# Kernel tuning notes

Hardware: AMD Instinct MI355X
Metric: run time of the kernel (lower is better)

## Reference

```python
import jax, jax.numpy as jnp
import numpy as np

B, S, D, K = 4, 4096, 1024, 64

def setup_inputs() -> dict:
    key = jax.random.key(0)
    kx, kq, kk, kv, ko = jax.random.split(key, 5)
    scale = 1.0 / np.sqrt(D)
    return {
        "x": jax.random.normal(kx, (B, S, D), dtype=jnp.float32),
        "Wq": jax.random.uniform(kq, (K, D), dtype=jnp.float32, minval=-scale, maxval=scale),
        "Wk": jax.random.uniform(kk, (K, D), dtype=jnp.float32, minval=-scale, maxval=scale),
        "Wv": jax.random.uniform(kv, (K, D), dtype=jnp.float32, minval=-scale, maxval=scale),
        "Wo": jax.random.uniform(ko, (D, K), dtype=jnp.float32, minval=-1.0/np.sqrt(K), maxval=1.0/np.sqrt(K)),
    }

def reference(x, Wq, Wk, Wv, Wo):
    # projections: torch Linear(dim, key_dim, bias=False) -> x @ W.T
    Q = jax.nn.elu(x @ Wq.T) + 1.0          # [B,S,K]
    Kf = jax.nn.elu(x @ Wk.T) + 1.0         # [B,S,K]
    V = x @ Wv.T                             # [B,S,K]
    # causal running KV state via cumsum of outer products: [B,S,K,K]
    KV_sum = jnp.cumsum(Kf[..., :, None] * V[..., None, :], axis=1)
    K_sum = jnp.cumsum(Kf, axis=1)           # [B,S,K]
    num = jnp.einsum('bsk,bskm->bsm', Q, KV_sum)   # [B,S,K]
    den = jnp.einsum('bsk,bsk->bs', Q, K_sum)[..., None]
    out = num / (den + 1e-6)
    return out @ Wo.T                         # [B,S,D]
```

## Files before the change

kernel.cpp:

```cpp
#include <hip/hip_runtime.h>

#define BB 4
#define SS 4096
#define DDIM 1024
#define KDIM 64
#define NCHUNK 64
#define TCHUNK 256
#define MROWS 16384

typedef short short8v __attribute__((ext_vector_type(8)));
typedef float f32x4 __attribute__((ext_vector_type(4)));
#define MFMA16 __builtin_amdgcn_mfma_f32_16x16x32_bf16

#define GLDS16(gp, lp) __builtin_amdgcn_global_load_lds( \
    (const __attribute__((address_space(1))) unsigned int*)(gp), \
    (__attribute__((address_space(3))) unsigned int*)(lp), 16, 0, 0)

__device__ __forceinline__ ushort f2bf(float f) {
    uint u = __float_as_uint(f);
    u += 0x7FFFu + ((u >> 16) & 1u);
    return (ushort)(u >> 16);
}

__device__ __forceinline__ uint cvtpk(float lo, float hi) {
    uint r;
    asm("v_cvt_pk_bf16_f32 %0, %1, %2" : "=v"(r) : "v"(lo), "v"(hi));
    return r;
}

__global__ __launch_bounds__(256) void k_wconv(
    const float* __restrict__ Wq, const float* __restrict__ Wk,
    const float* __restrict__ Wv, const float* __restrict__ Wo,
    ushort* __restrict__ Whf, ushort* __restrict__ Wof)
{
    const int b = blockIdx.x, t = threadIdx.x;
    const int ks = t >> 7;
    const int l = (t >> 1) & 63;
    const int half = t & 1;
    if (b < 192) {
        const int s = b / 12, cf = b % 12;
        const int grow = cf * 16 + (l & 15);
        const int gcol = s * 64 + ks * 32 + ((l >> 4) & 3) * 8 + half * 4;
        const float* src = (grow < 64) ? (Wq + (size_t)grow * DDIM)
                         : (grow < 128) ? (Wk + (size_t)(grow - 64) * DDIM)
                                        : (Wv + (size_t)(grow - 128) * DDIM);
        float4 v = *(const float4*)&src[gcol];
        ushort* dst = &Whf[(size_t)(((s * 12 + cf) * 2 + ks) * 64 + l) * 8 + half * 4];
        dst[0] = f2bf(v.x); dst[1] = f2bf(v.y); dst[2] = f2bf(v.z); dst[3] = f2bf(v.w);
    } else {
        const int cf = b - 192;
        const int d = cf * 16 + (l & 15);
        const int kc = ks * 32 + ((l >> 4) & 3) * 8 + half * 4;
        float4 v = *(const float4*)&Wo[(size_t)d * KDIM + kc];
        ushort* dst = &Wof[(size_t)((cf * 2 + ks) * 64 + l) * 8 + half * 4];
        dst[0] = f2bf(v.x); dst[1] = f2bf(v.y); dst[2] = f2bf(v.z); dst[3] = f2bf(v.w);
    }
}

#define EBP 216
__global__ __launch_bounds__(512, 2) void k_proj(
    const float* __restrict__ x, const ushort* __restrict__ Whf,
    ushort* __restrict__ Qf, ushort* __restrict__ Kff,
    ushort* __restrict__ KfT, ushort* __restrict__ VT)
{
    __shared__ float  ldsA[2][4096];
    __shared__ ushort ldsB[2][12288];
    const int t = threadIdx.x;
    const int w = t >> 6, l = t & 63;
    const int rw = w >> 2, cw = w & 3;
    const int g = blockIdx.x;
    const int row0 = g * 64;
    const int lq = l >> 4;

    auto stageX = [&](int s, int buf) {
#pragma unroll
        for (int ii = 0; ii < 2; ++ii) {
            const int i = w * 2 + ii;
            const int r = 4 * i + (l >> 4);
            const int sg = ((l & 15) >> 1) ^ (r & 7);
            const float* gp = &x[(size_t)(row0 + r) * DDIM + s * 64 + sg * 8 + (l & 1) * 4];
            GLDS16(gp, &ldsA[buf][i * 256]);
        }
    };
    auto stageW = [&](int s, int buf) {
#pragma unroll
        for (int ii = 0; ii < 3; ++ii) {
            const int f = w * 3 + ii;
            const ushort* gp = &Whf[(size_t)(s * 24 + f) * 512 + l * 8];
            GLDS16(gp, &ldsB[buf][f * 512]);
        }
    };

    f32x4 acc[2][3];
#pragma unroll
    for (int r = 0; r < 2; ++r)
#pragma unroll
        for (int c = 0; c < 3; ++c) acc[r][c] = (f32x4){0.f, 0.f, 0.f, 0.f};

    auto compute = [&](int buf) {
#pragma unroll
        for (int ks = 0; ks < 2; ++ks) {
            short8v a[2];
#pragma unroll
            for (int j = 0; j < 2; ++j) {
                const int r = (rw * 2 + j) * 16 + (l & 15);
                const int gs = (ks * 4 + (l >> 4)) ^ (l & 7);
                const float* ap = &ldsA[buf][r * 64 + gs * 8];
                float4 a0 = *(const float4*)ap;
                float4 a1 = *(const float4*)(ap + 4);
                uint4 pk;
                pk.x = cvtpk(a0.x, a0.y); pk.y = cvtpk(a0.z, a0.w);
                pk.z = cvtpk(a1.x, a1.y); pk.w = cvtpk(a1.z, a1.w);
                a[j] = *(short8v*)&pk;
            }
#pragma unroll
            for (int c = 0; c < 3; ++c) {
                short8v b = *(const short8v*)&ldsB[buf][(size_t)((cw * 3 + c) * 2 + ks) * 512 + l * 8];
                acc[0][c] = MFMA16(a[0], b, acc[0][c], 0, 0, 0);
                acc[1][c] = MFMA16(a[1], b, acc[1][c], 0, 0, 0);
            }
        }
    };

    stageX(0, 0); stageW(0, 0);
    __syncthreads();
    for (int s = 0; s < 16; ++s) {
        const int cur = s & 1, nxt = cur ^ 1;
        if (s < 15) { stageX(s + 1, nxt); stageW(s + 1, nxt); }
        compute(cur);
        __syncthreads();
    }

    ushort* eb = (ushort*)&ldsA[0][0];
#pragma unroll
    for (int rfi = 0; rfi < 2; ++rfi)
#pragma unroll
        for (int ci = 0; ci < 3; ++ci) {
            const int col = (cw * 3 + ci) * 16 + (l & 15);
#pragma unroll
            for (int q = 0; q < 4; ++q) {
                const int rl = (rw * 2 + rfi) * 16 + lq * 4 + q;
                float v = acc[rfi][ci][q];
                if (col < 128) v = (v > 0.f) ? v + 1.f : __expf(v);
                eb[rl * EBP + col] = f2bf(v);
            }
        }
    __syncthreads();

    {
        const int which = w >> 2, rh = (w >> 1) & 1, rfm = w & 1;
#pragma unroll
        for (int ks = 0; ks < 2; ++ks) {
            const int r = rh * 32 + rfm * 16 + (l & 15);
            const int c0 = ks * 32 + ((l >> 4) & 3) * 8 + (which ? 64 : 0);
            short8v v8 = *(const short8v*)&eb[r * EBP + c0];
            const size_t fo = ((size_t)((g * 2 + rh) * 4 + rfm * 2 + ks)) * 512 + l * 8;
            if (which == 0) *(short8v*)&Qf[fo] = v8;
            else            *(short8v*)&Kff[fo] = v8;
        }
    }
    {
        const int which = w >> 2, f = w & 3;
#pragma unroll
        for (int js = 0; js < 2; ++js) {
            const int col = (which ? 128 : 64) + f * 16 + (l & 15);
            const int jb = js * 32 + ((l >> 4) & 3) * 8;
            short8v tv;
#pragma unroll
            for (int e = 0; e < 8; ++e) tv[e] = (short)eb[(jb + e) * EBP + col];
            const size_t fo = ((size_t)(g * 8 + f * 2 + js)) * 512 + l * 8;
            if (which == 0) *(short8v*)&KfT[fo] = tv;
            else            *(short8v*)&VT[fo]  = tv;
        }
    }
}

__global__ __launch_bounds__(64) void k_chunksum(
    const ushort* __restrict__ KfT, const ushort* __restrict__ VT,
    float* __restrict__ KVc, float* __restrict__ Ksc)
{
    const int g = blockIdx.x, l = threadIdx.x;
    short8v ka[4][2], vb[4][2];
#pragma unroll
    for (int f = 0; f < 4; ++f)
#pragma unroll
        for (int js = 0; js < 2; ++js) {
            const size_t fo = ((size_t)(g * 8 + f * 2 + js)) * 512 + l * 8;
            ka[f][js] = *(const short8v*)&KfT[fo];
            vb[f][js] = *(const short8v*)&VT[fo];
        }
    short8v onesf;
#pragma unroll
    for (int e = 0; e < 8; ++e) onesf[e] = ((l & 15) == 0) ? (short)0x3F80 : (short)0;

    f32x4 acc[4][5];
#pragma unroll
    for (int kf = 0; kf < 4; ++kf)
#pragma unroll
        for (int mf = 0; mf < 5; ++mf) acc[kf][mf] = (f32x4){0.f, 0.f, 0.f, 0.f};
#pragma unroll
    for (int js = 0; js < 2; ++js)
#pragma unroll
        for (int kf = 0; kf < 4; ++kf) {
#pragma unroll
            for (int mf = 0; mf < 4; ++mf)
                acc[kf][mf] = MFMA16(ka[kf][js], vb[mf][js], acc[kf][mf], 0, 0, 0);
            acc[kf][4] = MFMA16(ka[kf][js], onesf, acc[kf][4], 0, 0, 0);
        }
    const int lq = l >> 4;
#pragma unroll
    for (int kf = 0; kf < 4; ++kf) {
#pragma unroll
        for (int q = 0; q < 4; ++q) {
            const int k = kf * 16 + lq * 4 + q;
#pragma unroll
            for (int mf = 0; mf < 4; ++mf)
                KVc[(size_t)g * 4096 + k * 64 + mf * 16 + (l & 15)] = acc[kf][mf][q];
            if ((l & 15) == 0) Ksc[(size_t)g * KDIM + k] = acc[kf][4][q];
        }
    }
}

__global__ void k_scan(const float* __restrict__ KVc, const float* __restrict__ Ksc,
                       float* __restrict__ Sst, float* __restrict__ Kss)
{
    const int b = blockIdx.x / 65;
    const int r = blockIdx.x % 65;
    const int t = threadIdx.x;
    if (r < 64) {
        const int e = r * 64 + t;
        float v[64];
#pragma unroll
        for (int i = 0; i < 64; ++i)
            v[i] = KVc[((size_t)(b * NCHUNK + i)) * 4096 + e];
        float acc = 0.f;
#pragma unroll
        for (int i = 0; i < 64; ++i) {
            Sst[((size_t)(b * NCHUNK + i)) * 4096 + e] = acc;
            acc += v[i];
        }
    } else {
        float v[64];
#pragma unroll
        for (int i = 0; i < 64; ++i)
            v[i] = Ksc[((size_t)(b * NCHUNK + i)) * KDIM + t];
        float acc = 0.f;
#pragma unroll
        for (int i = 0; i < 64; ++i) {
            Kss[((size_t)(b * NCHUNK + i)) * KDIM + t] = acc;
            acc += v[i];
        }
    }
}

__global__ __launch_bounds__(256) void k_intra(
    const ushort* __restrict__ Qf, const ushort* __restrict__ Kff,
    const ushort* __restrict__ VT, const float* __restrict__ Sst,
    const float* __restrict__ Kss, const ushort* __restrict__ Wof,
    float* __restrict__ out)
{
    __shared__ ushort pb[32 * 64];
    __shared__ ushort sT[80 * 64];
    __shared__ float ob[4][16 * 68 + 4];
    const int bx = blockIdx.x, t = threadIdx.x;
    const int g = bx >> 1, rh = bx & 1;
    const int w = t >> 6, l = t & 63;
    const int lq = l >> 4;

    {
        const int k = t >> 2, m0 = (t & 3) * 16;
        const float4* sp = (const float4*)&Sst[(size_t)g * 4096 + k * 64 + m0];
        float4 f0 = sp[0], f1 = sp[1], f2v = sp[2], f3 = sp[3];
        float fv[16] = {f0.x, f0.y, f0.z, f0.w, f1.x, f1.y, f1.z, f1.w,
                        f2v.x, f2v.y, f2v.z, f2v.w, f3.x, f3.y, f3.z, f3.w};
#pragma unroll
        for (int i = 0; i < 16; ++i) {
            const int m = m0 + i;
            sT[m * 64 + (k ^ ((m & 7) << 3))] = f2bf(fv[i]);
        }
        if (t < 64) sT[64 * 64 + t] = f2bf(Kss[(size_t)g * KDIM + t]);
        for (int idx = t; idx < 960; idx += 256) sT[65 * 64 + idx] = 0;
    }

    const int rf = w & 1;
    short8v qa[2];
#pragma unroll
    for (int ks = 0; ks < 2; ++ks)
        qa[ks] = *(const short8v*)&Qf[((size_t)((g * 2 + rh) * 4 + rf * 2 + ks)) * 512 + l * 8];
    {
        const int cfh = w >> 1;
        f32x4 accs[2];
#pragma unroll
        for (int ci = 0; ci < 2; ++ci) accs[ci] = (f32x4){0.f, 0.f, 0.f, 0.f};
#pragma unroll
        for (int ci = 0; ci < 2; ++ci) {
            const int cf = cfh * 2 + ci;
#pragma unroll
            for (int ks = 0; ks < 2; ++ks) {
                short8v kb = *(const short8v*)&Kff[((size_t)((g * 2 + (cf >> 1)) * 4 + (cf & 1) * 2 + ks)) * 512 + l * 8];
                accs[ci] = MFMA16(qa[ks], kb, accs[ci], 0, 0, 0);
            }
        }
#pragma unroll
        for (int ci = 0; ci < 2; ++ci)
#pragma unroll
            for (int q = 0; q < 4; ++q) {
                const int row = rf * 16 + lq * 4 + q;
                const int col = (cfh * 2 + ci) * 16 + (l & 15);
                const float sv = (col <= rh * 32 + row) ? accs[ci][q] : 0.f;
                pb[row * 64 + (col ^ ((row & 7) << 3))] = f2bf(sv);
            }
    }
    __syncthreads();

    const int mg = w >> 1;
    f32x4 an0 = (f32x4){0.f,0.f,0.f,0.f}, an1 = (f32x4){0.f,0.f,0.f,0.f};
    f32x4 ad = (f32x4){0.f,0.f,0.f,0.f};
    short8v onesf;
#pragma unroll
    for (int e = 0; e < 8; ++e) onesf[e] = ((l & 15) == 0) ? (short)0x3F80 : (short)0;
#pragma unroll
    for (int js = 0; js < 2; ++js) {
        const int prow = rf * 16 + (l & 15);
        const int pbase = js * 32 + ((l >> 4) & 3) * 8;
        short8v pa = *(const short8v*)&pb[prow * 64 + (pbase ^ ((prow & 7) << 3))];
        short8v v0 = *(const short8v*)&VT[((size_t)(g * 8 + (mg * 2 + 0) * 2 + js)) * 512 + l * 8];
        short8v v1 = *(const short8v*)&VT[((size_t)(g * 8 + (mg * 2 + 1) * 2 + js)) * 512 + l * 8];
        an0 = MFMA16(pa, v0, an0, 0, 0, 0);
        an1 = MFMA16(pa, v1, an1, 0, 0, 0);
        ad  = MFMA16(pa, onesf, ad, 0, 0, 0);
    }
#pragma unroll
    for (int ks = 0; ks < 2; ++ks) {
        const int base = ks * 32 + ((l >> 4) & 3) * 8;
        const int r0 = (mg * 2 + 0) * 16 + (l & 15);
        const int r1 = (mg * 2 + 1) * 16 + (l & 15);
        const int r4 = 64 + (l & 15);
        short8v s0 = *(const short8v*)&sT[r0 * 64 + (base ^ ((r0 & 7) << 3))];
        short8v s1 = *(const short8v*)&sT[r1 * 64 + (base ^ ((r1 & 7) << 3))];
        short8v s4 = *(const short8v*)&sT[r4 * 64 + (base ^ ((r4 & 7) << 3))];
        an0 = MFMA16(qa[ks], s0, an0, 0, 0, 0);
        an1 = MFMA16(qa[ks], s1, an1, 0, 0, 0);
        ad  = MFMA16(qa[ks], s4, ad, 0, 0, 0);
    }
#pragma unroll
    for (int q = 0; q < 4; ++q) {
        const float den = __shfl(ad[q], (l & 48));
        const float rinv = 1.f / (den + 1e-6f);
        const int row = rf * 16 + lq * 4 + q;
        const int c0 = (mg * 2 + 0) * 16 + (l & 15);
        const int c1 = (mg * 2 + 1) * 16 + (l & 15);
        pb[row * 64 + (c0 ^ ((row & 7) << 3))] = f2bf(an0[q] * rinv);
        pb[row * 64 + (c1 ^ ((row & 7) << 3))] = f2bf(an1[q] * rinv);
    }
    __syncthreads();

    short8v oa[2][2];
#pragma unroll
    for (int rfi = 0; rfi < 2; ++rfi)
#pragma unroll
        for (int ks = 0; ks < 2; ++ks) {
            const int row = rfi * 16 + (l & 15);
            const int base = ks * 32 + ((l >> 4) & 3) * 8;
            oa[rfi][ks] = *(const short8v*)&pb[row * 64 + (base ^ ((row & 7) << 3))];
        }
    float* obw = ob[w];
#pragma unroll
    for (int rr = 0; rr < 4; ++rr) {
        f32x4 acco[2][4];
#pragma unroll
        for (int rfi = 0; rfi < 2; ++rfi)
#pragma unroll
            for (int ci = 0; ci < 4; ++ci) acco[rfi][ci] = (f32x4){0.f, 0.f, 0.f, 0.f};
#pragma unroll
        for (int ci = 0; ci < 4; ++ci) {
            const int cfg = w * 16 + rr * 4 + ci;
#pragma unroll
            for (int ks = 0; ks < 2; ++ks) {
                short8v wb = *(const short8v*)&Wof[((size_t)(cfg * 2 + ks)) * 512 + l * 8];
#pragma unroll
                for (int rfi = 0; rfi < 2; ++rfi)
                    acco[rfi][ci] = MFMA16(oa[rfi][ks], wb, acco[rfi][ci], 0, 0, 0);
            }
        }
#pragma unroll
        for (int rfi = 0; rfi < 2; ++rfi) {
#pragma unroll
            for (int ci = 0; ci < 4; ++ci)
#pragma unroll
                for (int q = 0; q < 4; ++q)
                    obw[(lq * 4 + q) * 68 + ci * 16 + (l & 15)] = acco[rfi][ci][q];
#pragma unroll
            for (int rg = 0; rg < 4; ++rg) {
                const int row = rg * 4 + lq;
                float4 vv = *(const float4*)&obw[row * 68 + (l & 15) * 4];
                *(float4*)&out[((size_t)(g * 64 + rh * 32 + rfi * 16 + row)) * DDIM
                               + w * 256 + rr * 64 + (l & 15) * 4] = vv;
            }
        }
    }
}

extern "C" void kernel_launch(void* const* d_in, const int* in_sizes, int n_in,
                              void* d_out, int out_size, void* d_ws, size_t ws_size,
                              hipStream_t stream)
{
    const float* x  = (const float*)d_in[0];
    const float* Wq = (const float*)d_in[1];
    const float* Wk = (const float*)d_in[2];
    const float* Wv = (const float*)d_in[3];
    const float* Wo = (const float*)d_in[4];
    float* out = (float*)d_out;

    float* ws   = (float*)d_ws;
    float* KVc  = ws;
    float* Sst  = KVc + (size_t)TCHUNK * 4096;
    float* Ksc  = Sst + (size_t)TCHUNK * 4096;
    float* Kss  = Ksc + (size_t)TCHUNK * KDIM;
    ushort* Whf = (ushort*)(Kss + (size_t)TCHUNK * KDIM);
    ushort* Wof = Whf + (size_t)192 * DDIM;
    ushort* Qf  = Wof + (size_t)64 * 1024;
    ushort* Kff = Qf  + (size_t)512 * 4 * 512;
    ushort* KfT = Kff + (size_t)512 * 4 * 512;
    ushort* VT  = KfT + (size_t)256 * 8 * 512;

    k_wconv<<<dim3(256), dim3(256), 0, stream>>>(Wq, Wk, Wv, Wo, Whf, Wof);
    k_proj<<<dim3(TCHUNK), dim3(512), 0, stream>>>(x, Whf, Qf, Kff, KfT, VT);
    k_chunksum<<<dim3(TCHUNK), dim3(64), 0, stream>>>(KfT, VT, KVc, Ksc);
    k_scan<<<dim3(BB * 65), dim3(64), 0, stream>>>(KVc, Ksc, Sst, Kss);
    k_intra<<<dim3(TCHUNK * 2), dim3(256), 0, stream>>>(Qf, Kff, VT, Sst, Kss, Wof, out);
}
```

Measured before the change: 56.20 us.

## Halve projection row tile, convert x to bf16 at staging via register prefetch

The projection kernel now handles 32 rows per block instead of 64, which doubles the grid to 512 blocks for more parallelism across CUs. x is loaded into registers one stage ahead and converted to bf16 before being written to LDS in MFMA fragment layout, replacing direct global-to-LDS fp32 copies that were converted on every fragment read. LDS use shrinks to a single bf16 buffer, and the loop is unrolled with fixed ping-pong buffers. In exchange, each block now reads the weight tile for only half as many rows, which doubles weight traffic per row and halves MFMA reuse per wave.

```diff
diff --git a/kernel.cpp b/kernel.cpp
--- a/kernel.cpp
+++ b/kernel.cpp
@@ -63,115 +63,104 @@
     ushort* __restrict__ Qf, ushort* __restrict__ Kff,
     ushort* __restrict__ KfT, ushort* __restrict__ VT)
 {
-    __shared__ float  ldsA[2][4096];
-    __shared__ ushort ldsB[2][12288];
+    __shared__ ushort lds[2][14336];
     const int t = threadIdx.x;
     const int w = t >> 6, l = t & 63;
     const int rw = w >> 2, cw = w & 3;
-    const int g = blockIdx.x;
-    const int row0 = g * 64;
+    const int mb = blockIdx.x;
+    const int row0 = mb * 32;
     const int lq = l >> 4;
 
-    auto stageX = [&](int s, int buf) {
-#pragma unroll
-        for (int ii = 0; ii < 2; ++ii) {
-            const int i = w * 2 + ii;
-            const int r = 4 * i + (l >> 4);
-            const int sg = ((l & 15) >> 1) ^ (r & 7);
-            const float* gp = &x[(size_t)(row0 + r) * DDIM + s * 64 + sg * 8 + (l & 1) * 4];
-            GLDS16(gp, &ldsA[buf][i * 256]);
-        }
+    const int xr = t >> 4;
+    const int xc = (t & 15) * 4;
+    const float* xbase = &x[(size_t)(row0 + xr) * DDIM + xc];
+    const int xslot = (((xr >> 4) * 2 + (xc >> 5)) * 64
+                       + ((xr & 15) | (((xc >> 3) & 3) << 4))) * 8 + ((xc >> 2) & 1) * 4;
+
+    auto ldX = [&](int s) -> float4 { return *(const float4*)(xbase + s * 64); };
+    auto stX = [&](float4 v, int buf) {
+        uint2 pk;
+        pk.x = cvtpk(v.x, v.y);
+        pk.y = cvtpk(v.z, v.w);
+        *(uint2*)&lds[buf][xslot] = pk;
     };
     auto stageW = [&](int s, int buf) {
 #pragma unroll
         for (int ii = 0; ii < 3; ++ii) {
             const int f = w * 3 + ii;
             const ushort* gp = &Whf[(size_t)(s * 24 + f) * 512 + l * 8];
-            GLDS16(gp, &ldsB[buf][f * 512]);
+            GLDS16(gp, &lds[buf][2048 + f * 512]);
         }
     };
 
-    f32x4 acc[2][3];
-#pragma unroll
-    for (int r = 0; r < 2; ++r)
-#pragma unroll
-        for (int c = 0; c < 3; ++c) acc[r][c] = (f32x4){0.f, 0.f, 0.f, 0.f};
+    f32x4 acc[3];
+#pragma unroll
+    for (int c = 0; c < 3; ++c) acc[c] = (f32x4){0.f, 0.f, 0.f, 0.f};
 
     auto compute = [&](int buf) {
 #pragma unroll
         for (int ks = 0; ks < 2; ++ks) {
-            short8v a[2];
-#pragma unroll
-            for (int j = 0; j < 2; ++j) {
-                const int r = (rw * 2 + j) * 16 + (l & 15);
-                const int gs = (ks * 4 + (l >> 4)) ^ (l & 7);
-                const float* ap = &ldsA[buf][r * 64 + gs * 8];
-                float4 a0 = *(const float4*)ap;
-                float4 a1 = *(const float4*)(ap + 4);
-                uint4 pk;
-                pk.x = cvtpk(a0.x, a0.y); pk.y = cvtpk(a0.z, a0.w);
-                pk.z = cvtpk(a1.x, a1.y); pk.w = cvtpk(a1.z, a1.w);
-                a[j] = *(short8v*)&pk;
+            short8v a = *(const short8v*)&lds[buf][((rw * 2 + ks) * 64 + l) * 8];
+#pragma unroll
+            for (int c = 0; c < 3; ++c) {
+                short8v b = *(const short8v*)&lds[buf][2048 + ((cw * 3 + c) * 2 + ks) * 512 + l * 8];
+                acc[c] = MFMA16(a, b, acc[c], 0, 0, 0);
             }
-#pragma unroll
-            for (int c = 0; c < 3; ++c) {
-                short8v b = *(const short8v*)&ldsB[buf][(size_t)((cw * 3 + c) * 2 + ks) * 512 + l * 8];
-                acc[0][c] = MFMA16(a[0], b, acc[0][c], 0, 0, 0);
-                acc[1][c] = MFMA16(a[1], b, acc[1][c], 0, 0, 0);
-            }
         }
     };
 
-    stageX(0, 0); stageW(0, 0);
+    float4 xe = ldX(0);
+    float4 xo = ldX(1);
+    stageW(0, 0);
+    stX(xe, 0);
     __syncthreads();
-    for (int s = 0; s < 16; ++s) {
-        const int cur = s & 1, nxt = cur ^ 1;
-        if (s < 15) { stageX(s + 1, nxt); stageW(s + 1, nxt); }
-        compute(cur);
+#pragma unroll
+    for (int s2 = 0; s2 < 16; s2 += 2) {
+        if (s2 + 2 < 16) xe = ldX(s2 + 2);
+        if (s2 + 1 < 16) stageW(s2 + 1, 1);
+        compute(0);
+        if (s2 + 1 < 16) stX(xo, 1);
         __syncthreads();
-    }
-
-    ushort* eb = (ushort*)&ldsA[0][0];
-#pragma unroll
-    for (int rfi = 0; rfi < 2; ++rfi)
-#pragma unroll
-        for (int ci = 0; ci < 3; ++ci) {
-            const int col = (cw * 3 + ci) * 16 + (l & 15);
-#pragma unroll
-            for (int q = 0; q < 4; ++q) {
-                const int rl = (rw * 2 + rfi) * 16 + lq * 4 + q;
-                float v = acc[rfi][ci][q];
-                if (col < 128) v = (v > 0.f) ? v + 1.f : __expf(v);
-                eb[rl * EBP + col] = f2bf(v);
-            }
-        }
+        if (s2 + 3 < 16) xo = ldX(s2 + 3);
+        if (s2 + 2 < 16) stageW(s2 + 2, 0);
+        if (s2 + 1 < 16) compute(1);
+        if (s2 + 2 < 16) stX(xe, 0);
+        __syncthreads();
+    }
+
+    ushort* eb = &lds[0][0];
+#pragma unroll
+    for (int c = 0; c < 3; ++c) {
+        const int col = (cw * 3 + c) * 16 + (l & 15);
+#pragma unroll
+        for (int q = 0; q < 4; ++q) {
+            const int row = rw * 16 + lq * 4 + q;
+            float v = acc[c][q];
+            if (col < 128) v = (v > 0.f) ? v + 1.f : __expf(v);
+            eb[row * EBP + col] = f2bf(v);
+        }
+    }
     __syncthreads();
 
     {
-        const int which = w >> 2, rh = (w >> 1) & 1, rfm = w & 1;
-#pragma unroll
-        for (int ks = 0; ks < 2; ++ks) {
-            const int r = rh * 32 + rfm * 16 + (l & 15);
-            const int c0 = ks * 32 + ((l >> 4) & 3) * 8 + (which ? 64 : 0);
-            short8v v8 = *(const short8v*)&eb[r * EBP + c0];
-            const size_t fo = ((size_t)((g * 2 + rh) * 4 + rfm * 2 + ks)) * 512 + l * 8;
-            if (which == 0) *(short8v*)&Qf[fo] = v8;
-            else            *(short8v*)&Kff[fo] = v8;
-        }
+        const int which = w >> 2, rf = (w >> 1) & 1, ks = w & 1;
+        const int r = rf * 16 + (l & 15);
+        const int c0 = ks * 32 + ((l >> 4) & 3) * 8 + (which ? 64 : 0);
+        short8v v8 = *(const short8v*)&eb[r * EBP + c0];
+        const size_t fo = ((size_t)(mb * 4 + rf * 2 + ks)) * 512 + l * 8;
+        if (which == 0) *(short8v*)&Qf[fo] = v8;
+        else            *(short8v*)&Kff[fo] = v8;
     }
     {
         const int which = w >> 2, f = w & 3;
-#pragma unroll
-        for (int js = 0; js < 2; ++js) {
-            const int col = (which ? 128 : 64) + f * 16 + (l & 15);
-            const int jb = js * 32 + ((l >> 4) & 3) * 8;
-            short8v tv;
-#pragma unroll
-            for (int e = 0; e < 8; ++e) tv[e] = (short)eb[(jb + e) * EBP + col];
-            const size_t fo = ((size_t)(g * 8 + f * 2 + js)) * 512 + l * 8;
-            if (which == 0) *(short8v*)&KfT[fo] = tv;
-            else            *(short8v*)&VT[fo]  = tv;
-        }
+        const int col = (which ? 128 : 64) + f * 16 + (l & 15);
+        const int jb = ((l >> 4) & 3) * 8;
+        short8v tv;
+#pragma unroll
+        for (int e = 0; e < 8; ++e) tv[e] = (short)eb[(jb + e) * EBP + col];
+        const size_t fo = ((size_t)((mb >> 1) * 8 + f * 2 + (mb & 1))) * 512 + l * 8;
+        if (which == 0) *(short8v*)&KfT[fo] = tv;
+        else            *(short8v*)&VT[fo]  = tv;
     }
 }
 
@@ -425,7 +414,7 @@
     ushort* VT  = KfT + (size_t)256 * 8 * 512;
 
     k_wconv<<<dim3(256), dim3(256), 0, stream>>>(Wq, Wk, Wv, Wo, Whf, Wof);
-    k_proj<<<dim3(TCHUNK), dim3(512), 0, stream>>>(x, Whf, Qf, Kff, KfT, VT);
+    k_proj<<<dim3(MROWS / 32), dim3(512), 0, stream>>>(x, Whf, Qf, Kff, KfT, VT);
     k_chunksum<<<dim3(TCHUNK), dim3(64), 0, stream>>>(KfT, VT, KVc, Ksc);
     k_scan<<<dim3(BB * 65), dim3(64), 0, stream>>>(KVc, Ksc, Sst, Kss);
     k_intra<<<dim3(TCHUNK * 2), dim3(256), 0, stream>>>(Qf, Kff, VT, Sst, Kss, Wof, out);
```

Measured after the change: 52.09 us (median of 3 runs). 7.3% less time.
